# Kernel tuning notes

Hardware: AMD Instinct MI355X
Metric: run time of the kernel (lower is better)

The kernel has to match this reference:

```python
import jax, jax.numpy as jnp
import numpy as np

D = 2048
H = 16
DH = D // H
L = 512  # kv_latent_dim
LN_EPS = 1e-5


def setup_inputs() -> dict:
    key = jax.random.key(0)
    ks = jax.random.split(key, 8)
    s = 0.02  # weight init scale to keep logits in a sane range
    x = jax.random.normal(ks[0], (2, 2048, D), dtype=jnp.float32)
    W_q = jax.random.normal(ks[1], (D, D), dtype=jnp.float32) * s      # torch Linear weight [out,in]
    Wd_kv = jax.random.normal(ks[2], (L, D), dtype=jnp.float32) * s
    W_uv = jax.random.normal(ks[3], (D, L), dtype=jnp.float32) * s
    W_uk = jax.random.normal(ks[4], (D, L), dtype=jnp.float32) * s
    W_o = jax.random.normal(ks[5], (D, D), dtype=jnp.float32) * s
    gamma = jnp.ones((L,), dtype=jnp.float32)
    beta = jnp.zeros((L,), dtype=jnp.float32)
    return {"x": x, "W_q": W_q, "Wd_kv": Wd_kv, "W_uv": W_uv, "W_uk": W_uk,
            "W_o": W_o, "gamma": gamma, "beta": beta}


def _layernorm(h, gamma, beta):
    mu = jnp.mean(h, axis=-1, keepdims=True)
    var = jnp.mean(jnp.square(h - mu), axis=-1, keepdims=True)
    return (h - mu) * jax.lax.rsqrt(var + LN_EPS) * gamma + beta


def reference(x, W_q, Wd_kv, W_uv, W_uk, W_o, gamma, beta):
    B, S, _ = x.shape
    # absorbed K projection: (W_q @ W_uk) -> [H, dh, L]
    absorbed_k = (W_q @ W_uk).reshape(H, DH, L)
    # latent KV: layernorm(x @ Wd_kv^T), [B, S, L]
    c_kv = _layernorm(jnp.einsum('bsd,ld->bsl', x, Wd_kv), gamma, beta)
    S_full = c_kv.shape[1]
    # NOTE: original uses raw x (not W_q(x)) as q; W_q is folded into absorbed_k
    q = x.reshape(B, S, H, DH)
    tmp = jnp.einsum('bshd,hdl->bhsl', q, absorbed_k)              # [B,H,S,L]
    scores = jnp.einsum('bhsl,btl->bhst', tmp, c_kv) / np.sqrt(DH)  # [B,H,S,S_full]
    # causal mask (past_length=0)
    mask = jnp.tril(jnp.ones((S, S_full), dtype=bool), k=0)
    scores = jnp.where(mask[None, None], scores, -jnp.inf)
    attn = jax.nn.softmax(scores, axis=-1)
    v_full = jnp.einsum('btl,dl->btd', c_kv, W_uv).reshape(B, S_full, H, DH)
    ctx = jnp.einsum('bhst,bthd->bshd', attn, v_full).reshape(B, S, D)
    out = jnp.einsum('bsd,od->bso', ctx, W_o)
    return out, c_kv
```

## Files before the change

kernel.cpp:

```cpp
#include <hip/hip_runtime.h>
#include <hip/hip_bf16.h>
#include <cstdint>


typedef __bf16 bf16x8 __attribute__((ext_vector_type(8)));
typedef __bf16 bf16x4 __attribute__((ext_vector_type(4)));
typedef float  f32x4  __attribute__((ext_vector_type(4)));

#define GLOBAL_AS __attribute__((address_space(1)))
#define LDS_AS    __attribute__((address_space(3)))

__device__ __forceinline__ void gload_lds16(const void* g, void* l) {
    __builtin_amdgcn_global_load_lds((const GLOBAL_AS uint32_t*)g,
                                     (LDS_AS uint32_t*)l, 16, 0, 0);
}

__global__ void k_cast_all(const float* __restrict__ x, const float* __restrict__ wq,
                           const float* __restrict__ wdkv, const float* __restrict__ wuv,
                           const float* __restrict__ wo,
                           __bf16* __restrict__ xb, __bf16* __restrict__ wqb,
                           __bf16* __restrict__ wdkvb, __bf16* __restrict__ wuvb,
                           __bf16* __restrict__ wob) {
    long i = (long)blockIdx.x * blockDim.x + threadIdx.x;
    const float* src; __bf16* dst; long off;
    if (i < 1048576)      { src = x;    dst = xb;    off = i; }
    else if (i < 1572864) { src = wq;   dst = wqb;   off = i - 1048576; }
    else if (i < 1703936) { src = wdkv; dst = wdkvb; off = i - 1572864; }
    else if (i < 1835008) { src = wuv;  dst = wuvb;  off = i - 1703936; }
    else                  { src = wo;   dst = wob;   off = i - 1835008; }
    long e = off * 8;
    float4 a = *reinterpret_cast<const float4*>(src + e);
    float4 b = *reinterpret_cast<const float4*>(src + e + 4);
    bf16x8 r;
    r[0] = (__bf16)a.x; r[1] = (__bf16)a.y; r[2] = (__bf16)a.z; r[3] = (__bf16)a.w;
    r[4] = (__bf16)b.x; r[5] = (__bf16)b.y; r[6] = (__bf16)b.z; r[7] = (__bf16)b.w;
    *reinterpret_cast<bf16x8*>(dst + e) = r;
}

__global__ void k_transpose_wuk(const float* __restrict__ in, __bf16* __restrict__ out) {
    __shared__ float t[64][65];
    const int d0 = blockIdx.x * 64, l0 = blockIdx.y * 64;
    const int tid = threadIdx.x;
    const int r = tid >> 4, c = (tid & 15) * 4;
    #pragma unroll
    for (int rr = 0; rr < 64; rr += 16) {
        float4 v = *reinterpret_cast<const float4*>(&in[(long)(d0 + r + rr) * 512 + l0 + c]);
        t[r + rr][c] = v.x; t[r + rr][c + 1] = v.y;
        t[r + rr][c + 2] = v.z; t[r + rr][c + 3] = v.w;
    }
    __syncthreads();
    const int lr = tid >> 2, dc = (tid & 3) * 16;
    bf16x8 o0, o1;
    #pragma unroll
    for (int i = 0; i < 8; ++i) { o0[i] = (__bf16)t[dc + i][lr]; o1[i] = (__bf16)t[dc + 8 + i][lr]; }
    *reinterpret_cast<bf16x8*>(&out[(long)(l0 + lr) * 2048 + d0 + dc]) = o0;
    *reinterpret_cast<bf16x8*>(&out[(long)(l0 + lr) * 2048 + d0 + dc + 8]) = o1;
}

template <typename CT>
__global__ __launch_bounds__(256, 2) void k_gemm_bt(
    const __bf16* __restrict__ A, const __bf16* __restrict__ B, CT* __restrict__ C,
    int K, int lda, int ldb, int ldc,
    long aOffZ, long bOffZ, long cOffZ, float cmul)
{
    A += (long)blockIdx.z * aOffZ;
    B += (long)blockIdx.z * bOffZ;
    C += (long)blockIdx.z * cOffZ;
    __shared__ __bf16 Asm[128][64];
    __shared__ __bf16 Bsm[128][64];
    const int tid  = threadIdx.x;
    const int lane = tid & 63, wid = tid >> 6;
    const int wr = wid >> 1, wc = wid & 1;
    const int tm = blockIdx.x * 128, tn = blockIdx.y * 128;
    const int r16 = lane & 15, g = lane >> 4;

    const int srow  = lane >> 3;
    const int sslot = lane & 7;
    const int scol  = ((sslot ^ srow) * 8);

    f32x4 acc[4][4];
    #pragma unroll
    for (int m = 0; m < 4; ++m)
        #pragma unroll
        for (int n = 0; n < 4; ++n) acc[m][n] = (f32x4){0.f, 0.f, 0.f, 0.f};

    for (int kt = 0; kt < K; kt += 64) {
        __syncthreads();
        #pragma unroll
        for (int c2 = 0; c2 < 4; ++c2) {
            const int chunk = wid * 4 + c2;
            const int row   = chunk * 8 + srow;
            gload_lds16(&A[(long)(tm + row) * lda + kt + scol], &Asm[chunk * 8][0]);
            gload_lds16(&B[(long)(tn + row) * ldb + kt + scol], &Bsm[chunk * 8][0]);
        }
        __syncthreads();
        #pragma unroll
        for (int kk = 0; kk < 2; ++kk) {
            bf16x8 af[4], bfr[4];
            #pragma unroll
            for (int m = 0; m < 4; ++m) {
                const int row = wr * 64 + m * 16 + r16;
                af[m] = *reinterpret_cast<const bf16x8*>(
                    reinterpret_cast<const char*>(&Asm[0][0]) +
                    row * 128 + (((kk * 4 + g) ^ (row & 7)) * 16));
            }
            #pragma unroll
            for (int n = 0; n < 4; ++n) {
                const int row = wc * 64 + n * 16 + r16;
                bfr[n] = *reinterpret_cast<const bf16x8*>(
                    reinterpret_cast<const char*>(&Bsm[0][0]) +
                    row * 128 + (((kk * 4 + g) ^ (row & 7)) * 16));
            }
            #pragma unroll
            for (int m = 0; m < 4; ++m)
                #pragma unroll
                for (int n = 0; n < 4; ++n)
                    acc[m][n] = __builtin_amdgcn_mfma_f32_16x16x32_bf16(af[m], bfr[n], acc[m][n], 0, 0, 0);
        }
    }
    #pragma unroll
    for (int m = 0; m < 4; ++m) {
        #pragma unroll
        for (int n = 0; n < 4; ++n) {
            #pragma unroll
            for (int j = 0; j < 4; ++j) {
                const int row = tm + wr * 64 + m * 16 + g * 4 + j;
                const int col = tn + wc * 64 + n * 16 + r16;
                C[(long)row * ldc + col] = (CT)(acc[m][n][j] * cmul);
            }
        }
    }
}

__global__ void k_layernorm(const float* __restrict__ pre, const float* __restrict__ gamma,
                            const float* __restrict__ beta, float* __restrict__ out_f32,
                            __bf16* __restrict__ out_bf16) {
    const int row  = blockIdx.x * 4 + (threadIdx.x >> 6);
    const int lane = threadIdx.x & 63;
    const float* p = pre + (long)row * 512;
    float4 v0 = *reinterpret_cast<const float4*>(p + lane * 4);
    float4 v1 = *reinterpret_cast<const float4*>(p + 256 + lane * 4);
    float s  = v0.x + v0.y + v0.z + v0.w + v1.x + v1.y + v1.z + v1.w;
    float s2 = v0.x*v0.x + v0.y*v0.y + v0.z*v0.z + v0.w*v0.w
             + v1.x*v1.x + v1.y*v1.y + v1.z*v1.z + v1.w*v1.w;
    #pragma unroll
    for (int d = 1; d < 64; d <<= 1) { s += __shfl_xor(s, d); s2 += __shfl_xor(s2, d); }
    const float mu  = s * (1.0f / 512.0f);
    const float var = s2 * (1.0f / 512.0f) - mu * mu;
    const float rs  = rsqrtf(var + 1e-5f);
    float4 g0 = *reinterpret_cast<const float4*>(gamma + lane * 4);
    float4 g1 = *reinterpret_cast<const float4*>(gamma + 256 + lane * 4);
    float4 b0 = *reinterpret_cast<const float4*>(beta + lane * 4);
    float4 b1 = *reinterpret_cast<const float4*>(beta + 256 + lane * 4);
    float4 y0, y1;
    y0.x = (v0.x - mu) * rs * g0.x + b0.x;  y0.y = (v0.y - mu) * rs * g0.y + b0.y;
    y0.z = (v0.z - mu) * rs * g0.z + b0.z;  y0.w = (v0.w - mu) * rs * g0.w + b0.w;
    y1.x = (v1.x - mu) * rs * g1.x + b1.x;  y1.y = (v1.y - mu) * rs * g1.y + b1.y;
    y1.z = (v1.z - mu) * rs * g1.z + b1.z;  y1.w = (v1.w - mu) * rs * g1.w + b1.w;
    *reinterpret_cast<float4*>(out_f32 + (long)row * 512 + lane * 4) = y0;
    *reinterpret_cast<float4*>(out_f32 + (long)row * 512 + 256 + lane * 4) = y1;
    bf16x4 z0, z1;
    z0[0] = (__bf16)y0.x; z0[1] = (__bf16)y0.y; z0[2] = (__bf16)y0.z; z0[3] = (__bf16)y0.w;
    z1[0] = (__bf16)y1.x; z1[1] = (__bf16)y1.y; z1[2] = (__bf16)y1.z; z1[3] = (__bf16)y1.w;
    *reinterpret_cast<bf16x4*>(out_bf16 + (long)row * 512 + lane * 4) = z0;
    *reinterpret_cast<bf16x4*>(out_bf16 + (long)row * 512 + 256 + lane * 4) = z1;
}

__global__ __launch_bounds__(256, 2) void k_attn(
    const __bf16* __restrict__ xb,
    const __bf16* __restrict__ Keff,
    const __bf16* __restrict__ vT,
    __bf16* __restrict__ ctx)
{
    __shared__ __bf16 Ks[2][64][128];
    __shared__ __bf16 Vs[2][128][64];
    __shared__ __bf16 Pl[4][16][72];
    const int lane = threadIdx.x & 63;
    const int wid  = threadIdx.x >> 6;
    const int r16  = lane & 15;
    const int g    = lane >> 4;
    const int h = blockIdx.y, b = blockIdx.z;
    const int p = blockIdx.x;
    const int nkt = 32 - p;
    const int qbase[2] = { p * 64 + wid * 16, (31 - p) * 64 + wid * 16 };

    bf16x8 aQ[2][4];
    #pragma unroll
    for (int st = 0; st < 2; ++st) {
        const __bf16* qp = xb + ((long)(b * 2048 + qbase[st] + r16)) * 2048 + h * 128 + g * 8;
        #pragma unroll
        for (int ks = 0; ks < 4; ++ks)
            aQ[st][ks] = *reinterpret_cast<const bf16x8*>(qp + ks * 32);
    }

    f32x4 o[2][8];
    float mrow[2], lrow[2];
    #pragma unroll
    for (int st = 0; st < 2; ++st) {
        #pragma unroll
        for (int d8 = 0; d8 < 8; ++d8) o[st][d8] = (f32x4){0.f, 0.f, 0.f, 0.f};
        mrow[st] = -__builtin_inff(); lrow[st] = 0.f;
    }

    const __bf16* Kb = Keff + (long)h * (4096 * 128) + (long)b * (2048 * 128);
    const __bf16* Vb = vT + (long)h * (128 * 4096) + b * 2048;

    const int ksrow = wid * 4 + (lane >> 4);
    const int kslot = lane & 15;
    const int vsrow = wid * 8 + (lane >> 3);
    const int vslot = lane & 7;

    auto stage = [&](int kt, int buf) {
        const int k0s = kt * 64;
        #pragma unroll
        for (int c = 0; c < 4; ++c) {
            const int row = c * 16 + ksrow;
            const int gcol = ((kslot ^ (row & 15)) << 3);
            gload_lds16(&Kb[(long)(k0s + row) * 128 + gcol], &Ks[buf][c * 16 + wid * 4][0]);
        }
        #pragma unroll
        for (int c = 0; c < 4; ++c) {
            const int row = c * 32 + vsrow;
            const int gcol = ((vslot ^ (row & 7)) << 3);
            gload_lds16(&Vb[(long)row * 4096 + k0s + gcol], &Vs[buf][c * 32 + wid * 8][0]);
        }
    };

    const float THR = 11.541560327f;
    stage(0, 0);
    for (int kt = 0; kt < nkt; ++kt) {
        const int cur = kt & 1;
        const int k0 = kt * 64;
        __syncthreads();
        if (kt + 1 < nkt) stage(kt + 1, cur ^ 1);
        const char* Kbase = reinterpret_cast<const char*>(&Ks[cur][0][0]);
        const char* Vbase = reinterpret_cast<const char*>(&Vs[cur][0][0]);
        #pragma unroll
        for (int st = 0; st < 2; ++st) {
            if (st == 0 && kt > p) continue;
            f32x4 sT[4];
            #pragma unroll
            for (int kh = 0; kh < 4; ++kh) sT[kh] = (f32x4){0.f, 0.f, 0.f, 0.f};
            __builtin_amdgcn_s_setprio(1);
            #pragma unroll
            for (int kh = 0; kh < 4; ++kh) {
                const int krow = kh * 16 + r16;
                #pragma unroll
                for (int ks = 0; ks < 4; ++ks) {
                    bf16x8 bk = *reinterpret_cast<const bf16x8*>(
                        Kbase + krow * 256 + (((ks * 4 + g) ^ (krow & 15)) * 16));
                    sT[kh] = __builtin_amdgcn_mfma_f32_16x16x32_bf16(bk, aQ[st][ks], sT[kh], 0, 0, 0);
                }
            }
            __builtin_amdgcn_s_setprio(0);
            float sc[16];
            #pragma unroll
            for (int kh = 0; kh < 4; ++kh)
                #pragma unroll
                for (int j = 0; j < 4; ++j) sc[kh * 4 + j] = sT[kh][j];
            const bool diag = (st == 0) ? (kt == p) : (kt == nkt - 1);
            if (diag) {
                const int qabs = qbase[st] + r16;
                #pragma unroll
                for (int kh = 0; kh < 4; ++kh)
                    #pragma unroll
                    for (int j = 0; j < 4; ++j)
                        if (k0 + kh * 16 + g * 4 + j > qabs) sc[kh * 4 + j] = -1e30f;
            }
            float t01 = fmaxf(sc[0], sc[1]),  t23 = fmaxf(sc[2], sc[3]);
            float t45 = fmaxf(sc[4], sc[5]),  t67 = fmaxf(sc[6], sc[7]);
            float t89 = fmaxf(sc[8], sc[9]),  tab = fmaxf(sc[10], sc[11]);
            float tcd = fmaxf(sc[12], sc[13]), tef = fmaxf(sc[14], sc[15]);
            float tmax = fmaxf(fmaxf(fmaxf(t01, t23), fmaxf(t45, t67)),
                               fmaxf(fmaxf(t89, tab), fmaxf(tcd, tef)));
            tmax = fmaxf(tmax, __shfl_xor(tmax, 16));
            tmax = fmaxf(tmax, __shfl_xor(tmax, 32));
            const int needi = !__all(tmax <= mrow[st] + THR);
            float m = mrow[st], alpha = 1.f;
            if (needi) {
                const float mnew = fmaxf(m, tmax);
                alpha = __builtin_amdgcn_exp2f(m - mnew);
                m = mnew; mrow[st] = mnew;
            }
            float rsum = 0.f;
            bf16x4 pb[4];
            #pragma unroll
            for (int kh = 0; kh < 4; ++kh) {
                #pragma unroll
                for (int j = 0; j < 4; ++j) {
                    const float pv = __builtin_amdgcn_exp2f(sc[kh * 4 + j] - m);
                    rsum += pv;
                    pb[kh][j] = (__bf16)pv;
                }
            }
            rsum += __shfl_xor(rsum, 16);
            rsum += __shfl_xor(rsum, 32);
            lrow[st] = lrow[st] * alpha + rsum;
            #pragma unroll
            for (int kh = 0; kh < 4; ++kh)
                *reinterpret_cast<bf16x4*>(&Pl[wid][r16][kh * 16 + g * 4]) = pb[kh];
            if (needi) {
                float a4[4];
                #pragma unroll
                for (int j = 0; j < 4; ++j) a4[j] = __shfl(alpha, g * 4 + j);
                #pragma unroll
                for (int d8 = 0; d8 < 8; ++d8) {
                    o[st][d8][0] *= a4[0]; o[st][d8][1] *= a4[1];
                    o[st][d8][2] *= a4[2]; o[st][d8][3] *= a4[3];
                }
            }
            __builtin_amdgcn_s_setprio(1);
            #pragma unroll
            for (int kk = 0; kk < 2; ++kk) {
                bf16x8 pa = *reinterpret_cast<const bf16x8*>(&Pl[wid][r16][kk * 32 + g * 8]);
                #pragma unroll
                for (int d8 = 0; d8 < 8; ++d8) {
                    const int vrow = d8 * 16 + r16;
                    bf16x8 bv = *reinterpret_cast<const bf16x8*>(
                        Vbase + vrow * 128 + (((kk * 4 + g) ^ (vrow & 7)) * 16));
                    o[st][d8] = __builtin_amdgcn_mfma_f32_16x16x32_bf16(pa, bv, o[st][d8], 0, 0, 0);
                }
            }
            __builtin_amdgcn_s_setprio(0);
        }
    }
    #pragma unroll
    for (int st = 0; st < 2; ++st) {
        float rl4[4];
        #pragma unroll
        for (int j = 0; j < 4; ++j) rl4[j] = 1.0f / __shfl(lrow[st], g * 4 + j);
        #pragma unroll
        for (int d8 = 0; d8 < 8; ++d8) {
            #pragma unroll
            for (int j = 0; j < 4; ++j) {
                const int row = qbase[st] + g * 4 + j;
                ctx[((long)(b * 2048 + row)) * 2048 + h * 128 + d8 * 16 + r16] =
                    (__bf16)(o[st][d8][j] * rl4[j]);
            }
        }
    }
}

extern "C" void kernel_launch(void* const* d_in, const int* in_sizes, int n_in,
                              void* d_out, int out_size, void* d_ws, size_t ws_size,
                              hipStream_t stream) {
    const float* x     = (const float*)d_in[0];
    const float* W_q   = (const float*)d_in[1];
    const float* Wd_kv = (const float*)d_in[2];
    const float* W_uv  = (const float*)d_in[3];
    const float* W_uk  = (const float*)d_in[4];
    const float* W_o   = (const float*)d_in[5];
    const float* gamma = (const float*)d_in[6];
    const float* beta  = (const float*)d_in[7];
    float* out     = (float*)d_out;
    float* ckv_out = out + 8388608;

    char* ws = (char*)d_ws;
    __bf16* xb     = (__bf16*)(ws + 0);
    __bf16* Wqb    = (__bf16*)(ws + 16777216);
    __bf16* Wdkvb  = (__bf16*)(ws + 25165824);
    __bf16* Wuvb   = (__bf16*)(ws + 27262976);
    __bf16* Wob    = (__bf16*)(ws + 29360128);
    __bf16* WukT   = (__bf16*)(ws + 37748736);
    __bf16* absk   = (__bf16*)(ws + 39845888);
    float*  ckvpre = (float*) (ws + 41943040);
    __bf16* ckvb   = (__bf16*)(ws + 50331648);
    __bf16* Keff   = (__bf16*)(ws + 54525952);
    __bf16* vT     = (__bf16*)(ws + 71303168);
    __bf16* ctx    = (__bf16*)(ws + 88080384);

    k_cast_all<<<9216, 256, 0, stream>>>(x, W_q, Wd_kv, W_uv, W_o,
                                         xb, Wqb, Wdkvb, Wuvb, Wob);
    k_transpose_wuk<<<dim3(32, 8), 256, 0, stream>>>(W_uk, WukT);

    const float cscale = 1.4426950408889634f * 0.08838834764831845f;
    k_gemm_bt<__bf16><<<dim3(16, 4, 1), 256, 0, stream>>>(Wqb, WukT, absk,
        2048, 2048, 2048, 512, 0, 0, 0, cscale);
    k_gemm_bt<float><<<dim3(32, 4, 1), 256, 0, stream>>>(xb, Wdkvb, ckvpre,
        2048, 2048, 2048, 512, 0, 0, 0, 1.0f);
    k_layernorm<<<1024, 256, 0, stream>>>(ckvpre, gamma, beta, ckv_out, ckvb);
    k_gemm_bt<__bf16><<<dim3(32, 1, 16), 256, 0, stream>>>(ckvb, absk, Keff,
        512, 512, 512, 128, 0, 128 * 512, 4096 * 128, 1.0f);
    k_gemm_bt<__bf16><<<dim3(16, 32, 1), 256, 0, stream>>>(Wuvb, ckvb, vT,
        512, 512, 512, 4096, 0, 0, 0, 1.0f);
    k_attn<<<dim3(16, 16, 2), 256, 0, stream>>>(xb, Keff, vT, ctx);
    k_gemm_bt<float><<<dim3(32, 16, 1), 256, 0, stream>>>(ctx, Wob, out,
        2048, 2048, 2048, 2048, 0, 0, 0, 1.0f);
}
```

Baseline: 228.2 us.

## Add narrower GEMM tiles, remap attention grid, interleave two query strips

The GEMM kernel gains a warp-row template parameter, so the two small-N projection GEMMs run with 128x64 tiles and launch twice as many blocks, which fills more CUs. The attention launch becomes a 1D grid whose block index is swizzled so that neighbouring blocks share the same batch/head, with the aim of improving L2 reuse of K/V. Inside attention, each K fragment is loaded once and used for both query strips' score MFMAs, and the PV MFMAs for both strips are interleaved over shared V loads. This raises register pressure, and the interleaving adds branches on the light/heavy condition.

```diff
diff --git a/kernel.cpp b/kernel.cpp
--- a/kernel.cpp
+++ b/kernel.cpp
@@ -57,30 +57,35 @@
     *reinterpret_cast<bf16x8*>(&out[(long)(l0 + lr) * 2048 + d0 + dc + 8]) = o1;
 }
 
-template <typename CT>
+template <typename CT, int WR>
 __global__ __launch_bounds__(256, 2) void k_gemm_bt(
     const __bf16* __restrict__ A, const __bf16* __restrict__ B, CT* __restrict__ C,
     int K, int lda, int ldb, int ldc,
     long aOffZ, long bOffZ, long cOffZ, float cmul)
 {
+    constexpr int WC   = 4 / WR;
+    constexpr int BN   = WC * 64;
+    constexpr int WRB  = 128 / WR;
+    constexpr int MREP = WRB / 16;
+    constexpr int BCH  = BN / 32;
     A += (long)blockIdx.z * aOffZ;
     B += (long)blockIdx.z * bOffZ;
     C += (long)blockIdx.z * cOffZ;
     __shared__ __bf16 Asm[128][64];
-    __shared__ __bf16 Bsm[128][64];
+    __shared__ __bf16 Bsm[BN][64];
     const int tid  = threadIdx.x;
     const int lane = tid & 63, wid = tid >> 6;
-    const int wr = wid >> 1, wc = wid & 1;
-    const int tm = blockIdx.x * 128, tn = blockIdx.y * 128;
+    const int wr = wid / WC, wc = wid % WC;
+    const int tm = blockIdx.x * 128, tn = blockIdx.y * BN;
     const int r16 = lane & 15, g = lane >> 4;
 
     const int srow  = lane >> 3;
     const int sslot = lane & 7;
     const int scol  = ((sslot ^ srow) * 8);
 
-    f32x4 acc[4][4];
-    #pragma unroll
-    for (int m = 0; m < 4; ++m)
+    f32x4 acc[MREP][4];
+    #pragma unroll
+    for (int m = 0; m < MREP; ++m)
         #pragma unroll
         for (int n = 0; n < 4; ++n) acc[m][n] = (f32x4){0.f, 0.f, 0.f, 0.f};
 
@@ -91,15 +96,20 @@
             const int chunk = wid * 4 + c2;
             const int row   = chunk * 8 + srow;
             gload_lds16(&A[(long)(tm + row) * lda + kt + scol], &Asm[chunk * 8][0]);
+        }
+        #pragma unroll
+        for (int c2 = 0; c2 < BCH; ++c2) {
+            const int chunk = wid * BCH + c2;
+            const int row   = chunk * 8 + srow;
             gload_lds16(&B[(long)(tn + row) * ldb + kt + scol], &Bsm[chunk * 8][0]);
         }
         __syncthreads();
         #pragma unroll
         for (int kk = 0; kk < 2; ++kk) {
-            bf16x8 af[4], bfr[4];
-            #pragma unroll
-            for (int m = 0; m < 4; ++m) {
-                const int row = wr * 64 + m * 16 + r16;
+            bf16x8 af[MREP], bfr[4];
+            #pragma unroll
+            for (int m = 0; m < MREP; ++m) {
+                const int row = wr * WRB + m * 16 + r16;
                 af[m] = *reinterpret_cast<const bf16x8*>(
                     reinterpret_cast<const char*>(&Asm[0][0]) +
                     row * 128 + (((kk * 4 + g) ^ (row & 7)) * 16));
@@ -112,19 +122,19 @@
                     row * 128 + (((kk * 4 + g) ^ (row & 7)) * 16));
             }
             #pragma unroll
-            for (int m = 0; m < 4; ++m)
+            for (int m = 0; m < MREP; ++m)
                 #pragma unroll
                 for (int n = 0; n < 4; ++n)
                     acc[m][n] = __builtin_amdgcn_mfma_f32_16x16x32_bf16(af[m], bfr[n], acc[m][n], 0, 0, 0);
         }
     }
     #pragma unroll
-    for (int m = 0; m < 4; ++m) {
+    for (int m = 0; m < MREP; ++m) {
         #pragma unroll
         for (int n = 0; n < 4; ++n) {
             #pragma unroll
             for (int j = 0; j < 4; ++j) {
-                const int row = tm + wr * 64 + m * 16 + g * 4 + j;
+                const int row = tm + wr * WRB + m * 16 + g * 4 + j;
                 const int col = tn + wc * 64 + n * 16 + r16;
                 C[(long)row * ldc + col] = (CT)(acc[m][n][j] * cmul);
             }
@@ -179,8 +189,10 @@
     const int wid  = threadIdx.x >> 6;
     const int r16  = lane & 15;
     const int g    = lane >> 4;
-    const int h = blockIdx.y, b = blockIdx.z;
-    const int p = blockIdx.x;
+    const int bid  = blockIdx.x;
+    const int gidx = ((bid >> 7) << 3) | (bid & 7);
+    const int h = gidx & 15, b = gidx >> 4;
+    const int p = (bid >> 3) & 15;
     const int nkt = 32 - p;
     const int qbase[2] = { p * 64 + wid * 16, (31 - p) * 64 + wid * 16 };
 
@@ -235,30 +247,45 @@
         if (kt + 1 < nkt) stage(kt + 1, cur ^ 1);
         const char* Kbase = reinterpret_cast<const char*>(&Ks[cur][0][0]);
         const char* Vbase = reinterpret_cast<const char*>(&Vs[cur][0][0]);
-        #pragma unroll
-        for (int st = 0; st < 2; ++st) {
-            if (st == 0 && kt > p) continue;
-            f32x4 sT[4];
-            #pragma unroll
-            for (int kh = 0; kh < 4; ++kh) sT[kh] = (f32x4){0.f, 0.f, 0.f, 0.f};
-            __builtin_amdgcn_s_setprio(1);
-            #pragma unroll
-            for (int kh = 0; kh < 4; ++kh) {
-                const int krow = kh * 16 + r16;
-                #pragma unroll
-                for (int ks = 0; ks < 4; ++ks) {
-                    bf16x8 bk = *reinterpret_cast<const bf16x8*>(
-                        Kbase + krow * 256 + (((ks * 4 + g) ^ (krow & 15)) * 16));
-                    sT[kh] = __builtin_amdgcn_mfma_f32_16x16x32_bf16(bk, aQ[st][ks], sT[kh], 0, 0, 0);
-                }
-            }
-            __builtin_amdgcn_s_setprio(0);
+        const bool light = (kt <= p);
+
+        f32x4 sT[2][4];
+        #pragma unroll
+        for (int kh = 0; kh < 4; ++kh) {
+            sT[0][kh] = (f32x4){0.f, 0.f, 0.f, 0.f};
+            sT[1][kh] = (f32x4){0.f, 0.f, 0.f, 0.f};
+        }
+        __builtin_amdgcn_s_setprio(1);
+        #pragma unroll
+        for (int kh = 0; kh < 4; ++kh) {
+            const int krow = kh * 16 + r16;
+            bf16x8 bk[4];
+            #pragma unroll
+            for (int ks = 0; ks < 4; ++ks)
+                bk[ks] = *reinterpret_cast<const bf16x8*>(
+                    Kbase + krow * 256 + (((ks * 4 + g) ^ (krow & 15)) * 16));
+            #pragma unroll
+            for (int ks = 0; ks < 4; ++ks)
+                sT[1][kh] = __builtin_amdgcn_mfma_f32_16x16x32_bf16(bk[ks], aQ[1][ks], sT[1][kh], 0, 0, 0);
+            if (light) {
+                #pragma unroll
+                for (int ks = 0; ks < 4; ++ks)
+                    sT[0][kh] = __builtin_amdgcn_mfma_f32_16x16x32_bf16(bk[ks], aQ[0][ks], sT[0][kh], 0, 0, 0);
+            }
+        }
+        __builtin_amdgcn_s_setprio(0);
+
+        bf16x8 pa[2][2];
+        #pragma unroll
+        for (int sti = 0; sti < 2; ++sti) {
+            const int st = 1 - sti;
+            if (st == 0 && !light) continue;
+            const bool diag = (st == 0) ? (kt == p) : (kt == nkt - 1);
             float sc[16];
             #pragma unroll
             for (int kh = 0; kh < 4; ++kh)
                 #pragma unroll
-                for (int j = 0; j < 4; ++j) sc[kh * 4 + j] = sT[kh][j];
-            const bool diag = (st == 0) ? (kt == p) : (kt == nkt - 1);
+                for (int j = 0; j < 4; ++j) sc[kh * 4 + j] = sT[st][kh][j];
             if (diag) {
                 const int qabs = qbase[st] + r16;
                 #pragma unroll
@@ -299,6 +326,8 @@
             #pragma unroll
             for (int kh = 0; kh < 4; ++kh)
                 *reinterpret_cast<bf16x4*>(&Pl[wid][r16][kh * 16 + g * 4]) = pb[kh];
+            pa[st][0] = *reinterpret_cast<const bf16x8*>(&Pl[wid][r16][g * 8]);
+            pa[st][1] = *reinterpret_cast<const bf16x8*>(&Pl[wid][r16][32 + g * 8]);
             if (needi) {
                 float a4[4];
                 #pragma unroll
@@ -309,20 +338,22 @@
                     o[st][d8][2] *= a4[2]; o[st][d8][3] *= a4[3];
                 }
             }
-            __builtin_amdgcn_s_setprio(1);
-            #pragma unroll
-            for (int kk = 0; kk < 2; ++kk) {
-                bf16x8 pa = *reinterpret_cast<const bf16x8*>(&Pl[wid][r16][kk * 32 + g * 8]);
-                #pragma unroll
-                for (int d8 = 0; d8 < 8; ++d8) {
-                    const int vrow = d8 * 16 + r16;
-                    bf16x8 bv = *reinterpret_cast<const bf16x8*>(
-                        Vbase + vrow * 128 + (((kk * 4 + g) ^ (vrow & 7)) * 16));
-                    o[st][d8] = __builtin_amdgcn_mfma_f32_16x16x32_bf16(pa, bv, o[st][d8], 0, 0, 0);
-                }
-            }
-            __builtin_amdgcn_s_setprio(0);
-        }
+        }
+
+        __builtin_amdgcn_s_setprio(1);
+        #pragma unroll
+        for (int kk = 0; kk < 2; ++kk) {
+            #pragma unroll
+            for (int d8 = 0; d8 < 8; ++d8) {
+                const int vrow = d8 * 16 + r16;
+                bf16x8 bv = *reinterpret_cast<const bf16x8*>(
+                    Vbase + vrow * 128 + (((kk * 4 + g) ^ (vrow & 7)) * 16));
+                o[1][d8] = __builtin_amdgcn_mfma_f32_16x16x32_bf16(pa[1][kk], bv, o[1][d8], 0, 0, 0);
+                if (light)
+                    o[0][d8] = __builtin_amdgcn_mfma_f32_16x16x32_bf16(pa[0][kk], bv, o[0][d8], 0, 0, 0);
+            }
+        }
+        __builtin_amdgcn_s_setprio(0);
     }
     #pragma unroll
     for (int st = 0; st < 2; ++st) {
@@ -374,16 +405,16 @@
     k_transpose_wuk<<<dim3(32, 8), 256, 0, stream>>>(W_uk, WukT);
 
     const float cscale = 1.4426950408889634f * 0.08838834764831845f;
-    k_gemm_bt<__bf16><<<dim3(16, 4, 1), 256, 0, stream>>>(Wqb, WukT, absk,
+    k_gemm_bt<__bf16, 4><<<dim3(16, 8, 1), 256, 0, stream>>>(Wqb, WukT, absk,
         2048, 2048, 2048, 512, 0, 0, 0, cscale);
-    k_gemm_bt<float><<<dim3(32, 4, 1), 256, 0, stream>>>(xb, Wdkvb, ckvpre,
+    k_gemm_bt<float, 4><<<dim3(32, 8, 1), 256, 0, stream>>>(xb, Wdkvb, ckvpre,
         2048, 2048, 2048, 512, 0, 0, 0, 1.0f);
     k_layernorm<<<1024, 256, 0, stream>>>(ckvpre, gamma, beta, ckv_out, ckvb);
-    k_gemm_bt<__bf16><<<dim3(32, 1, 16), 256, 0, stream>>>(ckvb, absk, Keff,
+    k_gemm_bt<__bf16, 2><<<dim3(32, 1, 16), 256, 0, stream>>>(ckvb, absk, Keff,
         512, 512, 512, 128, 0, 128 * 512, 4096 * 128, 1.0f);
-    k_gemm_bt<__bf16><<<dim3(16, 32, 1), 256, 0, stream>>>(Wuvb, ckvb, vT,
+    k_gemm_bt<__bf16, 2><<<dim3(16, 32, 1), 256, 0, stream>>>(Wuvb, ckvb, vT,
         512, 512, 512, 4096, 0, 0, 0, 1.0f);
-    k_attn<<<dim3(16, 16, 2), 256, 0, stream>>>(xb, Keff, vT, ctx);
-    k_gemm_bt<float><<<dim3(32, 16, 1), 256, 0, stream>>>(ctx, Wob, out,
+    k_attn<<<512, 256, 0, stream>>>(xb, Keff, vT, ctx);
+    k_gemm_bt<float, 2><<<dim3(32, 16, 1), 256, 0, stream>>>(ctx, Wob, out,
         2048, 2048, 2048, 2048, 0, 0, 0, 1.0f);
 }
```

After: 215.8 us. -5.5%, faster.
